# Optimization experiments

Hardware: AMD Instinct MI355X
Metric: run time of the kernel (lower is better)

## Reference

```python
import jax, jax.numpy as jnp
import numpy as np

NUM_Q = 100000; NUM_C = 1000; D = 128; BS = 128; SEQ = 128
QN = 4; CN = 10; NQC = 4; AGG_HOPS = 2; RANK_K = 10
NEG = jnp.float32(-1e9)


def setup_inputs() -> dict:
    key = jax.random.key(0)
    ks = iter(jax.random.split(key, 40))
    def nrm(shape, scale=0.05):
        return jax.random.normal(next(ks), shape, dtype=jnp.float32) * scale
    inp = {}
    inp['question_seq'] = jax.random.randint(next(ks), (BS, SEQ), 0, NUM_Q, dtype=jnp.int32)
    inp['correct_seq'] = jax.random.randint(next(ks), (BS, SEQ), 0, 2, dtype=jnp.int32)
    inp['mask_seq'] = jnp.ones((BS, SEQ), dtype=jnp.int32)
    inp['question_neighbors'] = jax.random.randint(next(ks), (NUM_Q, QN), 0, NUM_C, dtype=jnp.int32)
    inp['concept_neighbors'] = jax.random.randint(next(ks), (NUM_C, CN), 0, NUM_Q, dtype=jnp.int32)
    inp['qc_table'] = jax.random.randint(next(ks), (NUM_Q, NQC), 0, NUM_C, dtype=jnp.int32)
    inp['Eq'] = nrm((NUM_Q, D), 1.0)
    inp['Ec'] = nrm((NUM_C, D), 1.0)
    inp['Er'] = nrm((2, D), 1.0)
    inp['W_ih1'] = nrm((3 * D, 2 * D)); inp['W_hh1'] = nrm((3 * D, D))
    inp['b_ih1'] = nrm((3 * D,)); inp['b_hh1'] = nrm((3 * D,))
    inp['W_ih2'] = nrm((3 * D, D)); inp['W_hh2'] = nrm((3 * D, D))
    inp['b_ih2'] = nrm((3 * D,)); inp['b_hh2'] = nrm((3 * D,))
    inp['W_agg'] = nrm((AGG_HOPS, D, D)); inp['b_agg'] = nrm((AGG_HOPS, D))
    inp['W_agg_last'] = nrm((D, D)); inp['b_agg_last'] = nrm((D,))
    inp['Wq'] = nrm((D, D)); inp['bq'] = nrm((D,))
    inp['Wk'] = nrm((D, D)); inp['bk'] = nrm((D,))
    inp['Ww'] = nrm((1, 2 * D)); inp['bw'] = nrm((1,))
    inp['h1_init'] = nrm((BS, D)); inp['h2_init'] = nrm((BS, D))
    return inp


def _gru(x, h, W_ih, W_hh, b_ih, b_hh):
    gi = x @ W_ih.T + b_ih
    gh = h @ W_hh.T + b_hh
    ir, iz, i_n = jnp.split(gi, 3, axis=-1)
    hr, hz, hn = jnp.split(gh, 3, axis=-1)
    r = jax.nn.sigmoid(ir + hr)
    z = jax.nn.sigmoid(iz + hz)
    n = jnp.tanh(i_n + r * hn)
    return (1 - z) * n + z * h


def _forward(question_seq, correct_seq, mask_seq, question_neighbors, concept_neighbors, qc_table,
             Eq, Ec, Er, W_ih1, W_hh1, b_ih1, b_hh1, W_ih2, W_hh2, b_ih2, b_hh2,
             W_agg, b_agg, W_agg_last, b_agg_last, Wq, bq, Wk, bk, Ww, bw, h1_init, h2_init):
    bs, seq_len = question_seq.shape
    d = Eq.shape[1]
    # detached question embeddings of the whole history (recap scoring key)
    K_all = jax.lax.stop_gradient(Eq[question_seq])  # [bs, seq, d]
    Wh, Wqc = Ww[:, :d], Ww[:, d:]  # MLP_W split over [state; question_concept]

    def predict(qc, hist, hist_mask):
        # qc: [bs,nqc,d], hist: [bs,ns,d], hist_mask: [bs,ns]
        Kp = qc @ Wk.T + bk                     # MLP_key
        Qp = hist @ Wq.T + bq                   # MLP_query
        logits = jnp.einsum('bsd,bqd->bsq', Qp, Kp)
        logits = jnp.where(hist_mask[:, :, None], logits, NEG)
        w = jax.nn.softmax(logits.reshape(bs, -1), axis=1)
        # pairwise sigmoid(MLP_W([h; e])) without materializing the concat
        v = jax.nn.sigmoid((hist @ Wh[0])[:, :, None] + (qc @ Wqc[0])[:, None, :] + bw[0])
        return jnp.sum(w * v.reshape(bs, -1), axis=1)

    def step(carry, t):
        h1, h2, state_hist, y_hat = carry
        q_t = jnp.take(question_seq, t, axis=1)
        r_t = jnp.take(correct_seq, t, axis=1)
        m_t = jnp.take(mask_seq, t, axis=1) != 0
        # --- 2-hop GNN aggregation (question -> concept -> question) ---
        n1 = question_neighbors[q_t]            # [bs, QN] concept ids
        n2 = concept_neighbors[n1]              # [bs, QN, CN] question ids
        emb = [Eq[q_t], Ec[n1], Eq[n2]]
        for i in range(AGG_HOPS):
            for j in range(AGG_HOPS - i):
                s = jnp.mean(emb[j + 1], axis=-2) + emb[j]
                emb[j] = jnp.tanh(s @ W_agg[j].T + b_agg[j])
        agg = jnp.tanh(emb[0] @ W_agg_last.T + b_agg_last)
        emb_q = jnp.where(m_t[:, None], agg, Eq[q_t])
        # --- GRU state updates (dropout in eval mode = identity) ---
        h1n = _gru(jnp.concatenate([emb_q, Er[r_t]], axis=1), h1, W_ih1, W_hh1, b_ih1, b_hh1)
        g2 = _gru(h1n, h2, W_ih2, W_hh2, b_ih2, b_hh2)
        # --- next question + its concepts ---
        q_next = jnp.take(question_seq, t + 1, axis=1)
        qc = jnp.concatenate([Eq[q_next][:, None], Ec[qc_table[q_next]]], axis=1)  # [bs, 1+NQC, d]
        # --- soft recap: top-k history states by detached embedding similarity ---
        scores = jnp.einsum('bsd,bd->bs', K_all, jax.lax.stop_gradient(Eq[q_next]))
        valid = jnp.arange(seq_len) < t
        scores = jnp.where(valid[None, :], scores, NEG)
        top_vals, top_idx = jax.lax.top_k(scores, RANK_K)
        sel = jnp.take_along_axis(state_hist, top_idx[:, :, None], axis=1)  # [bs, k, d]
        sel_mask = top_vals > NEG / 2
        hist = jnp.concatenate([g2[:, None], sel], axis=1)
        hist_mask = jnp.concatenate([jnp.ones((bs, 1), dtype=bool), sel_mask], axis=1)
        p = predict(qc, hist, hist_mask)
        idx = jnp.where(t == 0, 0, t + 1)  # original writes y_hat[:,0] at t==0
        y_hat = y_hat.at[:, idx].set(p)
        # h2 / state_history NOT updated at t==0 (original `continue`)
        upd = t > 0
        h2n = jnp.where(upd, g2, h2)
        state_hist = jnp.where(upd, state_hist.at[:, t].set(g2), state_hist)
        return (h1n, h2n, state_hist, y_hat), None

    init = (h1_init, h2_init,
            jnp.zeros((bs, seq_len, d), jnp.float32),
            jnp.zeros((bs, seq_len), jnp.float32))
    (_, _, _, y_hat), _ = jax.lax.scan(jax.checkpoint(step), init, jnp.arange(seq_len - 1))
    return y_hat


def reference(question_seq, correct_seq, mask_seq, question_neighbors, concept_neighbors, qc_table,
              Eq, Ec, Er, W_ih1, W_hh1, b_ih1, b_hh1, W_ih2, W_hh2, b_ih2, b_hh2,
              W_agg, b_agg, W_agg_last, b_agg_last, Wq, bq, Wk, bk, Ww, bw, h1_init, h2_init):
    return _forward(question_seq, correct_seq, mask_seq, question_neighbors, concept_neighbors, qc_table,
                    Eq, Ec, Er, W_ih1, W_hh1, b_ih1, b_hh1, W_ih2, W_hh2, b_ih2, b_hh2,
                    W_agg, b_agg, W_agg_last, b_agg_last, Wq, bq, Wk, bk, Ww, bw, h1_init, h2_init)
```

## Files before the change

### kernel.cpp

```cpp
#include <hip/hip_runtime.h>

#define DD 128
#define BSZ 128
#define SEQL 128
#define TST 127
#define QNN 4
#define CNN 10
#define NQCC 4
#define RKK 10
#define NEGV -1000000000.0f

#define OFF_WTA0    0
#define OFF_WTA1    16384
#define OFF_WTAL    32768
#define OFF_WTIH1A  49152
#define OFF_ERIH1   98304
#define OFF_MT      99072
#define OFF_WPACK   115456
#define OFF_ECA0    189184
#define OFF_E1C     317184
#define OFF_KQC     445184
#define OFF_VQCC    509184
#define OFF_KBC     510184
#define OFF_U       511184
#define OFF_W2      511312
#define OFF_C0      511440
#define OFF_GRAM    511488
#define OFF_GI1     511488
#define OFF_KQ0     6753792
#define OFF_VQC0    7802368
#define OFF_KB0     7818752
#define OFF_TIX     7835136
#define OFF_TMSK    7997696
#define OFF_CID     8160256

#define XI(e) ((e) + (((e) >> 5) << 2))

typedef __fp16 h2 __attribute__((ext_vector_type(2)));

__device__ __forceinline__ float sigm(float x) { return 1.0f / (1.0f + __expf(-x)); }
__device__ __forceinline__ unsigned pkh(float a, float b) {
  h2 v; v.x = (__fp16)a; v.y = (__fp16)b;
  return __builtin_bit_cast(unsigned, v);
}
__device__ __forceinline__ float fd2(float acc, unsigned w, h2 x) {
  return __builtin_amdgcn_fdot2(__builtin_bit_cast(h2, w), x, acc, false);
}
__device__ __forceinline__ float fd2u(float acc, unsigned w, unsigned x) {
  return __builtin_amdgcn_fdot2(__builtin_bit_cast(h2, w), __builtin_bit_cast(h2, x), acc, false);
}
__device__ __forceinline__ void bar() {
  asm volatile("s_waitcnt lgkmcnt(0)" ::: "memory");
  __builtin_amdgcn_s_barrier();
  asm volatile("" ::: "memory");
}

__global__ __launch_bounds__(256) void k_prep(
    const float* __restrict__ W_hh1, const float* __restrict__ W_ih2,
    const float* __restrict__ W_hh2, const float* __restrict__ W_agg,
    const float* __restrict__ W_agg_last, const float* __restrict__ W_ih1,
    const float* __restrict__ Er, float* __restrict__ ws) {
  int idx = blockIdx.x * 256 + threadIdx.x;
  const int TOT = 172800;
  for (int o = idx; o < TOT; o += gridDim.x * 256) {
    int r = o;
    if (r < 16384) { int j = r >> 7, i = r & 127; ws[OFF_WTA0 + r] = W_agg[i * 128 + j]; continue; }
    r -= 16384;
    if (r < 16384) { int j = r >> 7, i = r & 127; ws[OFF_WTA1 + r] = W_agg[16384 + i * 128 + j]; continue; }
    r -= 16384;
    if (r < 16384) { int j = r >> 7, i = r & 127; ws[OFF_WTAL + r] = W_agg_last[i * 128 + j]; continue; }
    r -= 16384;
    if (r < 49152) { int j = r / 384, i = r % 384; ws[OFF_WTIH1A + r] = W_ih1[i * 256 + j]; continue; }
    r -= 49152;
    if (r < 768) {
      int rr = r / 384, i2 = r % 384;
      float a = 0.f;
      for (int j = 0; j < 128; ++j) a += Er[rr * 128 + j] * W_ih1[i2 * 256 + 128 + j];
      ws[OFF_ERIH1 + r] = a; continue;
    }
    r -= 768;
    {
      int n = r & 3; int q = r >> 2;
      int i = q & 127; q >>= 7;
      int kk = q & 3; q >>= 2;
      int jc = q & 3; int c = q >> 2;
      int j0 = jc * 32 + kk * 8 + n * 2;
      const float* row;
      if (c < 3) row = W_hh1 + (size_t)(c * 128 + i) * 128;
      else if (c < 6) row = W_ih2 + (size_t)((c - 3) * 128 + i) * 128;
      else row = W_hh2 + (size_t)((c - 6) * 128 + i) * 128;
      ((unsigned*)ws)[OFF_WPACK + r] = pkh(row[j0], row[j0 + 1]);
    }
  }
}

__global__ __launch_bounds__(128) void k_mqk(
    const float* __restrict__ Wq, const float* __restrict__ Wk,
    const float* __restrict__ bq, const float* __restrict__ bk,
    float* __restrict__ ws) {
  int j = blockIdx.x;
  int tid = threadIdx.x;
  if (j < 128) {
    __shared__ float wkc[128];
    wkc[tid] = Wk[tid * 128 + j];
    __syncthreads();
    float a = 0.f;
    for (int l = 0; l < 128; ++l) a = fmaf(Wq[l * 128 + tid], wkc[l], a);
    ws[OFF_MT + j * 128 + tid] = a;
  } else if (j == 128) {
    float a = 0.f;
    for (int l = 0; l < 128; ++l) a = fmaf(Wq[l * 128 + tid], bk[l], a);
    ws[OFF_U + tid] = a;
  } else {
    float a = 0.f;
    for (int l = 0; l < 128; ++l) a = fmaf(bq[l], Wk[l * 128 + tid], a);
    ws[OFF_W2 + tid] = a;
    __shared__ float sc[128];
    sc[tid] = bq[tid] * bk[tid];
    __syncthreads();
    if (tid == 0) { float s = 0.f; for (int l = 0; l < 128; ++l) s += sc[l]; ws[OFF_C0] = s; }
  }
}

__global__ __launch_bounds__(128) void k_concept(
    const int* __restrict__ cnbr, const float* __restrict__ Eq,
    const float* __restrict__ Ec, const float* __restrict__ b_agg,
    const float* __restrict__ Ww, float* __restrict__ ws) {
  int c = blockIdx.x;
  int tid = threadIdx.x;
  __shared__ int s_nb[CNN];
  __shared__ float s_v[DD], s_ec[DD], s_t2[DD], s_w2[DD], s_kb2[DD];
  if (tid < CNN) s_nb[tid] = cnbr[c * CNN + tid];
  __syncthreads();
  float ec = Ec[c * DD + tid];
  float cm = 0.f;
#pragma unroll
  for (int l = 0; l < CNN; ++l) cm += Eq[(size_t)s_nb[l] * DD + tid];
  s_ec[tid] = ec;
  s_v[tid] = cm * 0.1f + ec;
  __syncthreads();
  const float* WtA0 = ws + OFF_WTA0;
  const float* WtA1 = ws + OFF_WTA1;
  const float* MT = ws + OFF_MT;
  float a1 = 0.f, a0 = 0.f, kq = 0.f;
#pragma unroll 8
  for (int j = 0; j < DD; ++j) {
    a1 += WtA1[j * DD + tid] * s_v[j];
    a0 += WtA0[j * DD + tid] * s_ec[j];
    kq += MT[j * DD + tid] * s_ec[j];
  }
  ws[OFF_E1C + c * DD + tid] = tanhf(a1 + b_agg[DD + tid]);
  ws[OFF_ECA0 + c * DD + tid] = a0;
  s_t2[tid] = kq + ws[OFF_U + tid];
  s_w2[tid] = s_ec[tid] * Ww[128 + tid];
  s_kb2[tid] = s_ec[tid] * ws[OFF_W2 + tid];
  __syncthreads();
  if (tid < 64) {
    ((unsigned*)ws)[OFF_KQC + c * 64 + tid] = pkh(s_t2[2 * tid], s_t2[2 * tid + 1]);
    float pa = s_w2[tid] + s_w2[tid + 64];
    float pb = s_kb2[tid] + s_kb2[tid + 64];
    for (int off = 32; off > 0; off >>= 1) { pa += __shfl_down(pa, off); pb += __shfl_down(pb, off); }
    if (tid == 0) { ws[OFF_VQCC + c] = pa; ws[OFF_KBC + c] = pb + ws[OFF_C0]; }
  }
}

__global__ __launch_bounds__(256) void k_gram(
    const int* __restrict__ qseq, const float* __restrict__ Eq,
    const float* __restrict__ Ww, float* __restrict__ ws) {
  int b = blockIdx.x;
  int tid = threadIdx.x;
  __shared__ float sX[128][129];
  __shared__ float s_tmp[2][8][DD];
  __shared__ int sq[SEQL];
  __shared__ float sU[DD], sWqc[DD], sW2[DD];
  if (tid < 128) {
    sq[tid] = qseq[b * SEQL + tid];
    sU[tid] = ws[OFF_U + tid];
    sWqc[tid] = Ww[128 + tid];
    sW2[tid] = ws[OFF_W2 + tid];
  }
  __syncthreads();
  for (int o = tid; o < 128 * 32; o += 256) {
    int s = o >> 5, p = o & 31;
    float4 v = ((const float4*)(Eq + (size_t)sq[s] * DD))[p];
    sX[s][p * 4] = v.x; sX[s][p * 4 + 1] = v.y; sX[s][p * 4 + 2] = v.z; sX[s][p * 4 + 3] = v.w;
  }
  __syncthreads();
  {
    int r0 = (tid >> 4) * 8, c0 = (tid & 15) * 8;
    float acc[8][8];
#pragma unroll
    for (int u = 0; u < 8; ++u)
#pragma unroll
      for (int v = 0; v < 8; ++v) acc[u][v] = 0.f;
    for (int k = 0; k < 128; ++k) {
      float a[8], bb[8];
#pragma unroll
      for (int u = 0; u < 8; ++u) { a[u] = sX[r0 + u][k]; bb[u] = sX[c0 + u][k]; }
#pragma unroll
      for (int u = 0; u < 8; ++u)
#pragma unroll
        for (int v = 0; v < 8; ++v) acc[u][v] = fmaf(a[u], bb[v], acc[u][v]);
    }
    float* gb = ws + OFF_GRAM + (size_t)b * 16384;
#pragma unroll
    for (int u = 0; u < 8; ++u) {
      float4 v0 = {acc[u][0], acc[u][1], acc[u][2], acc[u][3]};
      float4 v1 = {acc[u][4], acc[u][5], acc[u][6], acc[u][7]};
      ((float4*)(gb + (size_t)(r0 + u) * 128 + c0))[0] = v0;
      ((float4*)(gb + (size_t)(r0 + u) * 128 + c0 + 4))[0] = v1;
    }
  }
  {
    const float* MT = ws + OFF_MT;
    unsigned* KQ0 = (unsigned*)ws + OFF_KQ0;
    int i = tid & 127, half = tid >> 7;
    int s0 = half * 64;
    for (int sb = 0; sb < 64; sb += 8) {
      float acc[8];
#pragma unroll
      for (int u = 0; u < 8; ++u) acc[u] = 0.f;
      for (int j = 0; j < DD; ++j) {
        float w = MT[j * DD + i];
#pragma unroll
        for (int u = 0; u < 8; ++u) acc[u] = fmaf(w, sX[s0 + sb + u][j], acc[u]);
      }
      __syncthreads();
#pragma unroll
      for (int u = 0; u < 8; ++u) s_tmp[half][u][i] = acc[u] + sU[i];
      __syncthreads();
      for (int o = tid; o < 16 * 64; o += 256) {
        int rr = o >> 6, e = o & 63;
        int hh = rr >> 3, uu = rr & 7;
        int s = hh * 64 + sb + uu;
        KQ0[((size_t)b * 128 + s) * 64 + e] = pkh(s_tmp[hh][uu][2 * e], s_tmp[hh][uu][2 * e + 1]);
      }
      __syncthreads();
    }
  }
  if (tid < 128) {
    float a = 0.f, kb = 0.f;
    for (int j = 0; j < DD; ++j) {
      float xv = sX[tid][j];
      a = fmaf(xv, sWqc[j], a);
      kb = fmaf(xv, sW2[j], kb);
    }
    ws[OFF_VQC0 + b * 128 + tid] = a;
    ws[OFF_KB0 + b * 128 + tid] = kb + ws[OFF_C0];
  }
}

__global__ __launch_bounds__(128) void k_topk(
    const int* __restrict__ qseq, const int* __restrict__ qctab,
    float* __restrict__ ws) {
  int* tix = (int*)(ws + OFF_TIX);
  int* tmsk = (int*)(ws + OFF_TMSK);
  int* cid = (int*)(ws + OFF_CID);
  int tid = threadIdx.x;
  int lane = tid & 63, wv = tid >> 6;
  int bt = blockIdx.x * 2 + wv;
  int b = bt / TST, t = bt - b * TST;
  if (lane < 5) {
    int qn = qseq[b * SEQL + t + 1];
    cid[(b * 128 + t + 1) * 5 + lane] = (lane == 0) ? qn : qctab[qn * NQCC + lane - 1];
  }
  const float* grow = ws + OFF_GRAM + ((size_t)b * 128 + (t + 1)) * 128;
  float v0 = (lane < t) ? grow[lane] : NEGV;
  float v1 = (lane + 64 < t) ? grow[lane + 64] : NEGV;
  for (int k = 0; k < RKK; ++k) {
    float bv = v0; int bi = lane;
    if (v1 > bv) { bv = v1; bi = lane + 64; }
    for (int off = 32; off > 0; off >>= 1) {
      float ov = __shfl_down(bv, off);
      int oi = __shfl_down(bi, off);
      if (ov > bv || (ov == bv && oi < bi)) { bv = ov; bi = oi; }
    }
    bv = __shfl(bv, 0); bi = __shfl(bi, 0);
    if (lane == 0) {
      tix[bt * RKK + k] = bi;
      tmsk[bt * RKK + k] = (bv > NEGV * 0.5f) ? 1 : 0;
    }
    if (bi == lane) v0 = -__builtin_inff();
    if (bi == lane + 64) v1 = -__builtin_inff();
  }
}

__global__ __launch_bounds__(128) void k_agg(
    const int* __restrict__ qseq, const int* __restrict__ rseq,
    const int* __restrict__ mseq, const int* __restrict__ qnbr,
    const float* __restrict__ Eq, const float* __restrict__ b_agg,
    const float* __restrict__ b_agg_last, const float* __restrict__ b_ih1,
    float* __restrict__ ws) {
  int blk = blockIdx.x;
  int b = blk >> 4, g = blk & 15;
  int t0 = g * 8;
  int nu = (t0 + 8 <= TST) ? 8 : (TST - t0);
  int tid = threadIdx.x;
  __shared__ float s_a[8][DD], s_b[8][DD], s_c[8][DD];
  __shared__ int s_q[8], s_r[8], s_m[8];
  __shared__ int s_n1[8][QNN];
  if (tid < 8) {
    int ok = tid < nu;
    int idx = b * SEQL + (ok ? (t0 + tid) : 0);
    s_q[tid] = qseq[idx];
    s_r[tid] = ok ? rseq[idx] : 0;
    s_m[tid] = ok ? mseq[idx] : 0;
  }
  __syncthreads();
  if (tid < 32) { int u = tid >> 2, k = tid & 3; s_n1[u][k] = qnbr[s_q[u] * QNN + k]; }
  for (int o = tid; o < 8 * 32; o += 128) {
    int u = o >> 5, p = o & 31;
    float4 v = ((const float4*)(Eq + (size_t)s_q[u] * DD))[p];
    s_a[u][p * 4] = v.x; s_a[u][p * 4 + 1] = v.y; s_a[u][p * 4 + 2] = v.z; s_a[u][p * 4 + 3] = v.w;
  }
  __syncthreads();
  const float* WtA0 = ws + OFF_WTA0;
  const float* WtAL = ws + OFF_WTAL;
  const float* WtIH1A = ws + OFF_WTIH1A;
  const float* EcA0 = ws + OFF_ECA0;
  const float* E1C = ws + OFF_E1C;
  float acc[8];
#pragma unroll
  for (int u = 0; u < 8; ++u) acc[u] = 0.f;
  for (int j = 0; j < DD; ++j) {
    float w = WtA0[j * DD + tid];
#pragma unroll
    for (int u = 0; u < 8; ++u) acc[u] = fmaf(w, s_a[u][j], acc[u]);
  }
  float bat = b_agg[tid];
#pragma unroll
  for (int u = 0; u < 8; ++u) {
    int n0 = s_n1[u][0], n1 = s_n1[u][1], n2 = s_n1[u][2], n3 = s_n1[u][3];
    float pre0 = 0.25f * (EcA0[n0 * DD + tid] + EcA0[n1 * DD + tid] + EcA0[n2 * DD + tid] + EcA0[n3 * DD + tid]);
    float e0 = tanhf(acc[u] + pre0 + bat);
    float e1m = 0.25f * (E1C[n0 * DD + tid] + E1C[n1 * DD + tid] + E1C[n2 * DD + tid] + E1C[n3 * DD + tid]);
    s_b[u][tid] = e1m + e0;
  }
  __syncthreads();
#pragma unroll
  for (int u = 0; u < 8; ++u) acc[u] = 0.f;
  for (int j = 0; j < DD; ++j) {
    float w = WtA0[j * DD + tid];
#pragma unroll
    for (int u = 0; u < 8; ++u) acc[u] = fmaf(w, s_b[u][j], acc[u]);
  }
#pragma unroll
  for (int u = 0; u < 8; ++u) s_c[u][tid] = tanhf(acc[u] + bat);
  __syncthreads();
#pragma unroll
  for (int u = 0; u < 8; ++u) acc[u] = 0.f;
  for (int j = 0; j < DD; ++j) {
    float w = WtAL[j * DD + tid];
#pragma unroll
    for (int u = 0; u < 8; ++u) acc[u] = fmaf(w, s_c[u][j], acc[u]);
  }
  float balt = b_agg_last[tid];
#pragma unroll
  for (int u = 0; u < 8; ++u) {
    float aggv = tanhf(acc[u] + balt);
    s_b[u][tid] = s_m[u] ? aggv : s_a[u][tid];
  }
  __syncthreads();
  float g0[8], g1[8], g2[8];
#pragma unroll
  for (int u = 0; u < 8; ++u) { g0[u] = 0.f; g1[u] = 0.f; g2[u] = 0.f; }
  for (int j = 0; j < DD; ++j) {
    float w0 = WtIH1A[j * 384 + tid];
    float w1 = WtIH1A[j * 384 + 128 + tid];
    float w2 = WtIH1A[j * 384 + 256 + tid];
#pragma unroll
    for (int u = 0; u < 8; ++u) {
      float x = s_b[u][j];
      g0[u] = fmaf(w0, x, g0[u]);
      g1[u] = fmaf(w1, x, g1[u]);
      g2[u] = fmaf(w2, x, g2[u]);
    }
  }
  for (int u = 0; u < nu; ++u) {
    const float* ErI = ws + OFF_ERIH1 + s_r[u] * 384;
    float* gi1 = ws + OFF_GI1 + (size_t)(b * TST + t0 + u) * 384;
    gi1[tid] = g0[u] + ErI[tid] + b_ih1[tid];
    gi1[128 + tid] = g1[u] + ErI[128 + tid] + b_ih1[128 + tid];
    gi1[256 + tid] = g2[u] + ErI[256 + tid] + b_ih1[256 + tid];
  }
}

__global__ __launch_bounds__(512, 2) void k_seq(
    const float* __restrict__ b_hh1, const float* __restrict__ b_ih2,
    const float* __restrict__ b_hh2, const float* __restrict__ Ww,
    const float* __restrict__ bw, const float* __restrict__ h1i,
    const float* __restrict__ h2i, float* __restrict__ ws,
    float* __restrict__ out) {
  const int tid = threadIdx.x;
  const int b = blockIdx.x;
  const int i = tid >> 2, jc = tid & 3;
  const int lane = tid & 63, wv = tid >> 6;
  const int bt0 = b * TST;

  const float4* gi1f4 = (const float4*)(ws + OFF_GI1);
  const unsigned* KQ0 = (const unsigned*)ws + OFF_KQ0;
  const unsigned* KQC = (const unsigned*)ws + OFF_KQC;
  const float* vqc0_all = ws + OFF_VQC0;
  const float* vqcC_all = ws + OFF_VQCC;
  const float* kb0_all = ws + OFF_KB0;
  const float* kbC_all = ws + OFF_KBC;
  const int* tix_all = (const int*)(ws + OFF_TIX);
  const int* tmsk_all = (const int*)(ws + OFF_TMSK);
  const int* cid_all = (const int*)(ws + OFF_CID);
  const uint4* wp = (const uint4*)((const unsigned*)ws + OFF_WPACK);

  __shared__ float s_h1[144], s_h2[144], s_h1n[144], s_g2[144];
  __shared__ unsigned qph_pk[SEQL * 66];
  __shared__ unsigned s_Kq[5 * 66];
  __shared__ float s_gi1[384];
  __shared__ float s_vhh[SEQL];
  __shared__ float s_logit[64];
  __shared__ float s_bhh1[384], s_bih2[384], s_bhh2[384];
  __shared__ float s_vh[11], s_vqc[2][5], s_kb[2][5], s_bw;
  __shared__ int s_tix[RKK], s_hm[11], s_cidn[5];

  uint4 wgt[9][4];
#pragma unroll
  for (int c = 0; c < 9; ++c)
#pragma unroll
    for (int kk = 0; kk < 4; ++kk)
      wgt[c][kk] = wp[((c * 4 + jc) * 4 + kk) * 128 + i];
#pragma unroll
  for (int c = 0; c < 9; ++c)
#pragma unroll
    for (int kk = 0; kk < 4; ++kk)
      asm volatile("" : "+v"(wgt[c][kk].x), "+v"(wgt[c][kk].y),
                        "+v"(wgt[c][kk].z), "+v"(wgt[c][kk].w));

  if (tid < 384) { s_bhh1[tid] = b_hh1[tid]; s_bih2[tid] = b_ih2[tid]; s_bhh2[tid] = b_hh2[tid]; }
  if (tid < 128) { s_h1[XI(tid)] = h1i[b * DD + tid]; s_h2[XI(tid)] = h2i[b * DD + tid]; s_vhh[tid] = 0.f; }
  if (tid >= 55 && tid < 64) s_logit[tid] = NEGV;
  float wh_lo = 0.f, wh_hi = 0.f;
  if (wv == 7) { wh_lo = Ww[lane]; wh_hi = Ww[64 + lane]; }
  if (tid == 0) { s_bw = bw[0]; out[b * SEQL + 1] = 0.f; s_hm[0] = 1; }
  if (tid >= 296 && tid < 301) s_cidn[tid - 296] = cid_all[(b * 128 + 1) * 5 + tid - 296];
  if (tid >= 304 && tid < 314) s_tix[tid - 304] = tix_all[bt0 * RKK + tid - 304];
  if (tid >= 320 && tid < 330) s_hm[1 + tid - 320] = tmsk_all[bt0 * RKK + tid - 320];
  __syncthreads();
  for (int o = tid; o < SEQL * 66; o += 512) qph_pk[o] = 0u;
  if (tid < 96) ((float4*)s_gi1)[tid] = gi1f4[(size_t)bt0 * 96 + tid];
  else if (tid < 256) {
    int kx = tid - 96;
    { int s = kx >> 6, e = kx & 63;
      s_Kq[s * 66 + e] = (s == 0) ? KQ0[(size_t)(b * 128 + 1) * 64 + e] : KQC[s_cidn[s] * 64 + e]; }
    { int kx2 = kx + 160; int s = kx2 >> 6, e = kx2 & 63;
      s_Kq[s * 66 + e] = KQC[s_cidn[s] * 64 + e]; }
  } else if (tid < 266) {
    int k = tid - 256;
    if (k < 5) s_vqc[0][k] = (k == 0) ? vqc0_all[b * 128 + 1] : vqcC_all[s_cidn[k]];
    else { int s = k - 5; s_kb[0][s] = (s == 0) ? kb0_all[b * 128 + 1] : kbC_all[s_cidn[s]]; }
  }
  __syncthreads();
  if (tid < 5) s_cidn[tid] = cid_all[(b * 128 + 2) * 5 + tid];
  __syncthreads();

  for (int t = 0; t < TST; ++t) {
    const int par = t & 1, parn = par ^ 1;
    const int tpn = (t + 1 < TST) ? t + 1 : TST - 1;
    const int tpp = (t + 2 < TST) ? t + 2 : TST - 1;
    float4 pf4 = {0.f, 0.f, 0.f, 0.f};
    unsigned pfu = 0, pfu2 = 0; int pfs = 0; float pfv = 0.f, pfkb = 0.f;

    if (tid < 96) pf4 = gi1f4[(size_t)(bt0 + tpn) * 96 + tid];
    else if (tid < 256) {
      int kx = tid - 96;
      { int s = kx >> 6, e = kx & 63;
        pfu = (s == 0) ? KQ0[(size_t)(b * 128 + tpn + 1) * 64 + e] : KQC[s_cidn[s] * 64 + e]; }
      { int kx2 = kx + 160; int s = kx2 >> 6, e = kx2 & 63;
        pfu2 = KQC[s_cidn[s] * 64 + e]; }
    } else if (tid < 291) {
      int k = tid - 256;
      if (k < 5) pfv = (k == 0) ? vqc0_all[b * 128 + tpn + 1] : vqcC_all[s_cidn[k]];
      else if (k < 10) { int s = k - 5; pfkb = (s == 0) ? kb0_all[b * 128 + tpn + 1] : kbC_all[s_cidn[s]]; }
      else if (k < 20) pfs = tix_all[(bt0 + tpn) * RKK + k - 10];
      else if (k < 30) pfs = tmsk_all[(bt0 + tpn) * RKK + k - 20];
      else pfs = cid_all[(b * 128 + tpp + 1) * 5 + k - 30];
    }
    {
      const float4* xp = (const float4*)s_h1 + jc * 9;
      float a0 = 0.f, a1 = 0.f, a2 = 0.f;
#pragma unroll
      for (int kk = 0; kk < 4; ++kk) {
        float4 x0 = xp[2 * kk], x1 = xp[2 * kk + 1];
        h2 p0 = __builtin_amdgcn_cvt_pkrtz(x0.x, x0.y);
        h2 p1 = __builtin_amdgcn_cvt_pkrtz(x0.z, x0.w);
        h2 p2 = __builtin_amdgcn_cvt_pkrtz(x1.x, x1.y);
        h2 p3 = __builtin_amdgcn_cvt_pkrtz(x1.z, x1.w);
        uint4 w;
        w = wgt[0][kk]; a0 = fd2(a0, w.x, p0); a0 = fd2(a0, w.y, p1); a0 = fd2(a0, w.z, p2); a0 = fd2(a0, w.w, p3);
        w = wgt[1][kk]; a1 = fd2(a1, w.x, p0); a1 = fd2(a1, w.y, p1); a1 = fd2(a1, w.z, p2); a1 = fd2(a1, w.w, p3);
        w = wgt[2][kk]; a2 = fd2(a2, w.x, p0); a2 = fd2(a2, w.y, p1); a2 = fd2(a2, w.z, p2); a2 = fd2(a2, w.w, p3);
      }
      a0 += __shfl_down(a0, 2); a0 += __shfl_down(a0, 1);
      a1 += __shfl_down(a1, 2); a1 += __shfl_down(a1, 1);
      a2 += __shfl_down(a2, 2); a2 += __shfl_down(a2, 1);
      if (jc == 0) {
        float r = sigm(s_gi1[i] + a0 + s_bhh1[i]);
        float z = sigm(s_gi1[128 + i] + a1 + s_bhh1[128 + i]);
        float n = tanhf(s_gi1[256 + i] + r * (a2 + s_bhh1[256 + i]));
        s_h1n[XI(i)] = (1.f - z) * n + z * s_h1[XI(i)];
      }
    }
    bar();

    {
      const float4* xn = (const float4*)s_h1n + jc * 9;
      const float4* xh = (const float4*)s_h2 + jc * 9;
      float a0 = 0.f, a1 = 0.f, a2 = 0.f, c0 = 0.f, c1 = 0.f, c2 = 0.f;
#pragma unroll
      for (int kk = 0; kk < 4; ++kk) {
        float4 n0 = xn[2 * kk], n1 = xn[2 * kk + 1];
        h2 p0 = __builtin_amdgcn_cvt_pkrtz(n0.x, n0.y);
        h2 p1 = __builtin_amdgcn_cvt_pkrtz(n0.z, n0.w);
        h2 p2 = __builtin_amdgcn_cvt_pkrtz(n1.x, n1.y);
        h2 p3 = __builtin_amdgcn_cvt_pkrtz(n1.z, n1.w);
        float4 h0 = xh[2 * kk], h1v = xh[2 * kk + 1];
        h2 q0 = __builtin_amdgcn_cvt_pkrtz(h0.x, h0.y);
        h2 q1 = __builtin_amdgcn_cvt_pkrtz(h0.z, h0.w);
        h2 q2 = __builtin_amdgcn_cvt_pkrtz(h1v.x, h1v.y);
        h2 q3 = __builtin_amdgcn_cvt_pkrtz(h1v.z, h1v.w);
        uint4 w;
        w = wgt[3][kk]; a0 = fd2(a0, w.x, p0); a0 = fd2(a0, w.y, p1); a0 = fd2(a0, w.z, p2); a0 = fd2(a0, w.w, p3);
        w = wgt[4][kk]; a1 = fd2(a1, w.x, p0); a1 = fd2(a1, w.y, p1); a1 = fd2(a1, w.z, p2); a1 = fd2(a1, w.w, p3);
        w = wgt[5][kk]; a2 = fd2(a2, w.x, p0); a2 = fd2(a2, w.y, p1); a2 = fd2(a2, w.z, p2); a2 = fd2(a2, w.w, p3);
        w = wgt[6][kk]; c0 = fd2(c0, w.x, q0); c0 = fd2(c0, w.y, q1); c0 = fd2(c0, w.z, q2); c0 = fd2(c0, w.w, q3);
        w = wgt[7][kk]; c1 = fd2(c1, w.x, q0); c1 = fd2(c1, w.y, q1); c1 = fd2(c1, w.z, q2); c1 = fd2(c1, w.w, q3);
        w = wgt[8][kk]; c2 = fd2(c2, w.x, q0); c2 = fd2(c2, w.y, q1); c2 = fd2(c2, w.z, q2); c2 = fd2(c2, w.w, q3);
      }
      a0 += __shfl_down(a0, 2); a0 += __shfl_down(a0, 1);
      a1 += __shfl_down(a1, 2); a1 += __shfl_down(a1, 1);
      a2 += __shfl_down(a2, 2); a2 += __shfl_down(a2, 1);
      c0 += __shfl_down(c0, 2); c0 += __shfl_down(c0, 1);
      c1 += __shfl_down(c1, 2); c1 += __shfl_down(c1, 1);
      c2 += __shfl_down(c2, 2); c2 += __shfl_down(c2, 1);
      if (jc == 0) {
        float r = sigm(a0 + s_bih2[i] + c0 + s_bhh2[i]);
        float z = sigm(a1 + s_bih2[128 + i] + c1 + s_bhh2[128 + i]);
        float n = tanhf(a2 + s_bih2[256 + i] + r * (c2 + s_bhh2[256 + i]));
        s_g2[XI(i)] = (1.f - z) * n + z * s_h2[XI(i)];
      }
    }
    bar();

    if (tid < 440) {
      int p = tid >> 3, sub = tid & 7;
      int q = p / 5, s = p - q * 5;
      const unsigned* kpr = &s_Kq[s * 66 + sub * 8];
      float a = 0.f;
      if (q == 0) {
        int e0 = sub * 16;
#pragma unroll
        for (int k = 0; k < 8; ++k) {
          int e = XI(e0 + 2 * k);
          h2 x = __builtin_amdgcn_cvt_pkrtz(s_g2[e], s_g2[e + 1]);
          a = fd2(a, kpr[k], x);
        }
      } else {
        const unsigned* ro = qph_pk + s_tix[q - 1] * 66;
#pragma unroll
        for (int k = 0; k < 8; ++k) a = fd2u(a, ro[sub * 8 + k], kpr[k]);
      }
      a += __shfl_down(a, 4);
      a += __shfl_down(a, 2);
      a += __shfl_down(a, 1);
      if (sub == 0) s_logit[p] = s_hm[q] ? (a + s_kb[par][s]) : NEGV;
    } else if (wv == 7) {
      float pa = s_g2[XI(lane)] * wh_lo + s_g2[XI(64 + lane)] * wh_hi;
      for (int off = 32; off > 0; off >>= 1) pa += __shfl_down(pa, off);
      if (lane == 0) s_vh[0] = pa;
      if (lane >= 16 && lane < 26) s_vh[1 + lane - 16] = s_vhh[s_tix[lane - 16]];
    }
    bar();

    if (wv == 7) {
      float l = s_logit[lane];
      float m = l;
      for (int off = 32; off > 0; off >>= 1) m = fmaxf(m, __shfl_xor(m, off));
      float e = __expf(l - m);
      float v = 0.f;
      if (lane < 55) {
        int q = lane / 5, s = lane - q * 5;
        v = sigm(s_vh[q] + s_vqc[par][s] + s_bw);
      }
      float num = e * v, den = e;
      for (int off = 32; off > 0; off >>= 1) { num += __shfl_xor(num, off); den += __shfl_xor(den, off); }
      if (lane == 0) out[b * SEQL + ((t == 0) ? 0 : (t + 1))] = num / den;
    } else {
      if (tid < 96) ((float4*)s_gi1)[tid] = pf4;
      else if (tid < 256) {
        int kx = tid - 96;
        { int s = kx >> 6, e = kx & 63; s_Kq[s * 66 + e] = pfu; }
        { int kx2 = kx + 160; int s = kx2 >> 6, e = kx2 & 63; s_Kq[s * 66 + e] = pfu2; }
      } else if (tid < 291) {
        int k = tid - 256;
        if (k < 5) s_vqc[parn][k] = pfv;
        else if (k < 10) s_kb[parn][k - 5] = pfkb;
        else if (k < 20) s_tix[k - 10] = pfs;
        else if (k < 30) s_hm[1 + k - 20] = pfs;
        else s_cidn[k - 30] = pfs;
      }
      if (tid >= 320 && tid < 448) {
        int ii = tid - 320;
        s_h1[XI(ii)] = s_h1n[XI(ii)];
        if (t > 0) s_h2[XI(ii)] = s_g2[XI(ii)];
      }
      if (t > 0 && tid >= 96 && tid < 160) {
        int k2 = tid - 96;
        int e = XI(2 * k2);
        qph_pk[t * 66 + k2] = pkh(s_g2[e], s_g2[e + 1]);
      }
      if (tid == 0 && t > 0) s_vhh[t] = s_vh[0];
    }
    bar();
  }
}

extern "C" void kernel_launch(void* const* d_in, const int* in_sizes, int n_in,
                              void* d_out, int out_size, void* d_ws, size_t ws_size,
                              hipStream_t stream) {
  (void)in_sizes; (void)n_in; (void)out_size; (void)ws_size;
  const int* qseq = (const int*)d_in[0];
  const int* rseq = (const int*)d_in[1];
  const int* mseq = (const int*)d_in[2];
  const int* qnbr = (const int*)d_in[3];
  const int* cnbr = (const int*)d_in[4];
  const int* qctab = (const int*)d_in[5];
  const float* Eq = (const float*)d_in[6];
  const float* Ec = (const float*)d_in[7];
  const float* Er = (const float*)d_in[8];
  const float* W_ih1 = (const float*)d_in[9];
  const float* W_hh1 = (const float*)d_in[10];
  const float* b_ih1 = (const float*)d_in[11];
  const float* b_hh1 = (const float*)d_in[12];
  const float* W_ih2 = (const float*)d_in[13];
  const float* W_hh2 = (const float*)d_in[14];
  const float* b_ih2 = (const float*)d_in[15];
  const float* b_hh2 = (const float*)d_in[16];
  const float* W_agg = (const float*)d_in[17];
  const float* b_agg = (const float*)d_in[18];
  const float* W_agg_last = (const float*)d_in[19];
  const float* b_agg_last = (const float*)d_in[20];
  const float* Wq = (const float*)d_in[21];
  const float* bq = (const float*)d_in[22];
  const float* Wk = (const float*)d_in[23];
  const float* bk = (const float*)d_in[24];
  const float* Ww = (const float*)d_in[25];
  const float* bw = (const float*)d_in[26];
  const float* h1i = (const float*)d_in[27];
  const float* h2i = (const float*)d_in[28];
  float* ws = (float*)d_ws;
  float* out = (float*)d_out;

  hipLaunchKernelGGL(k_prep, dim3(675), dim3(256), 0, stream,
                     W_hh1, W_ih2, W_hh2, W_agg, W_agg_last, W_ih1, Er, ws);
  hipLaunchKernelGGL(k_mqk, dim3(130), dim3(128), 0, stream,
                     Wq, Wk, bq, bk, ws);
  hipLaunchKernelGGL(k_concept, dim3(1000), dim3(128), 0, stream,
                     cnbr, Eq, Ec, b_agg, Ww, ws);
  hipLaunchKernelGGL(k_gram, dim3(BSZ), dim3(256), 0, stream,
                     qseq, Eq, Ww, ws);
  hipLaunchKernelGGL(k_topk, dim3(BSZ * TST / 2), dim3(128), 0, stream,
                     qseq, qctab, ws);
  hipLaunchKernelGGL(k_agg, dim3(BSZ * 16), dim3(128), 0, stream,
                     qseq, rseq, mseq, qnbr, Eq, b_agg, b_agg_last, b_ih1, ws);
  hipLaunchKernelGGL(k_seq, dim3(BSZ), dim3(512), 0, stream,
                     b_hh1, b_ih2, b_hh2, Ww, bw, h1i, h2i, ws, out);
}
```

Baseline: 655.6 us.

## Software-pipeline attention/readout stage one step behind GRU to drop a barrier

```diff
diff --git a/kernel.cpp b/kernel.cpp
--- a/kernel.cpp
+++ b/kernel.cpp
@@ -409,9 +409,10 @@
   const int* cid_all = (const int*)(ws + OFF_CID);
   const uint4* wp = (const uint4*)((const unsigned*)ws + OFF_WPACK);
 
-  __shared__ float s_h1[144], s_h2[144], s_h1n[144], s_g2[144];
+  __shared__ float s_h1[144], s_h2[144], s_h1n[144];
+  __shared__ float s_g2[2][144];
   __shared__ unsigned qph_pk[SEQL * 66];
-  __shared__ unsigned s_Kq[5 * 66];
+  __shared__ unsigned s_Kq[2][5 * 66];
   __shared__ float s_gi1[384];
   __shared__ float s_vhh[SEQL];
   __shared__ float s_logit[64];
@@ -439,49 +440,33 @@
   if (wv == 7) { wh_lo = Ww[lane]; wh_hi = Ww[64 + lane]; }
   if (tid == 0) { s_bw = bw[0]; out[b * SEQL + 1] = 0.f; s_hm[0] = 1; }
   if (tid >= 296 && tid < 301) s_cidn[tid - 296] = cid_all[(b * 128 + 1) * 5 + tid - 296];
-  if (tid >= 304 && tid < 314) s_tix[tid - 304] = tix_all[bt0 * RKK + tid - 304];
-  if (tid >= 320 && tid < 330) s_hm[1 + tid - 320] = tmsk_all[bt0 * RKK + tid - 320];
   __syncthreads();
   for (int o = tid; o < SEQL * 66; o += 512) qph_pk[o] = 0u;
   if (tid < 96) ((float4*)s_gi1)[tid] = gi1f4[(size_t)bt0 * 96 + tid];
-  else if (tid < 256) {
-    int kx = tid - 96;
-    { int s = kx >> 6, e = kx & 63;
-      s_Kq[s * 66 + e] = (s == 0) ? KQ0[(size_t)(b * 128 + 1) * 64 + e] : KQC[s_cidn[s] * 64 + e]; }
-    { int kx2 = kx + 160; int s = kx2 >> 6, e = kx2 & 63;
-      s_Kq[s * 66 + e] = KQC[s_cidn[s] * 64 + e]; }
-  } else if (tid < 266) {
-    int k = tid - 256;
-    if (k < 5) s_vqc[0][k] = (k == 0) ? vqc0_all[b * 128 + 1] : vqcC_all[s_cidn[k]];
-    else { int s = k - 5; s_kb[0][s] = (s == 0) ? kb0_all[b * 128 + 1] : kbC_all[s_cidn[s]]; }
-  }
-  __syncthreads();
-  if (tid < 5) s_cidn[tid] = cid_all[(b * 128 + 2) * 5 + tid];
-  __syncthreads();
-
-  for (int t = 0; t < TST; ++t) {
+  __syncthreads();
+
+  for (int t = 0; t <= TST; ++t) {
     const int par = t & 1, parn = par ^ 1;
-    const int tpn = (t + 1 < TST) ? t + 1 : TST - 1;
-    const int tpp = (t + 2 < TST) ? t + 2 : TST - 1;
     float4 pf4 = {0.f, 0.f, 0.f, 0.f};
     unsigned pfu = 0, pfu2 = 0; int pfs = 0; float pfv = 0.f, pfkb = 0.f;
 
-    if (tid < 96) pf4 = gi1f4[(size_t)(bt0 + tpn) * 96 + tid];
-    else if (tid < 256) {
-      int kx = tid - 96;
-      { int s = kx >> 6, e = kx & 63;
-        pfu = (s == 0) ? KQ0[(size_t)(b * 128 + tpn + 1) * 64 + e] : KQC[s_cidn[s] * 64 + e]; }
-      { int kx2 = kx + 160; int s = kx2 >> 6, e = kx2 & 63;
-        pfu2 = KQC[s_cidn[s] * 64 + e]; }
-    } else if (tid < 291) {
-      int k = tid - 256;
-      if (k < 5) pfv = (k == 0) ? vqc0_all[b * 128 + tpn + 1] : vqcC_all[s_cidn[k]];
-      else if (k < 10) { int s = k - 5; pfkb = (s == 0) ? kb0_all[b * 128 + tpn + 1] : kbC_all[s_cidn[s]]; }
-      else if (k < 20) pfs = tix_all[(bt0 + tpn) * RKK + k - 10];
-      else if (k < 30) pfs = tmsk_all[(bt0 + tpn) * RKK + k - 20];
-      else pfs = cid_all[(b * 128 + tpp + 1) * 5 + k - 30];
-    }
-    {
+    if (t < TST) {
+      const int tg = (t + 1 < TST) ? t + 1 : TST - 1;
+      if (tid < 96) pf4 = gi1f4[(size_t)(bt0 + tg) * 96 + tid];
+      else if (tid < 256) {
+        int kx = tid - 96;
+        { int s = kx >> 6, e = kx & 63;
+          pfu = (s == 0) ? KQ0[(size_t)(b * 128 + t + 1) * 64 + e] : KQC[s_cidn[s] * 64 + e]; }
+        { int kx2 = kx + 160; int s = kx2 >> 6, e = kx2 & 63;
+          pfu2 = KQC[s_cidn[s] * 64 + e]; }
+      } else if (tid < 291) {
+        int k = tid - 256;
+        if (k < 5) pfv = (k == 0) ? vqc0_all[b * 128 + t + 1] : vqcC_all[s_cidn[k]];
+        else if (k < 10) { int s = k - 5; pfkb = (s == 0) ? kb0_all[b * 128 + t + 1] : kbC_all[s_cidn[s]]; }
+        else if (k < 20) pfs = tix_all[(bt0 + t) * RKK + k - 10];
+        else if (k < 30) pfs = tmsk_all[(bt0 + t) * RKK + k - 20];
+        else { int tn = (t + 1 < TST) ? t + 1 : TST - 1; pfs = cid_all[(b * 128 + tn + 1) * 5 + k - 30]; }
+      }
       const float4* xp = (const float4*)s_h1 + jc * 9;
       float a0 = 0.f, a1 = 0.f, a2 = 0.f;
 #pragma unroll
@@ -506,11 +491,42 @@
         s_h1n[XI(i)] = (1.f - z) * n + z * s_h1[XI(i)];
       }
     }
+    if (t >= 1) {
+      if (tid < 440) {
+        int p = tid >> 3, sub = tid & 7;
+        int q = p / 5, s = p - q * 5;
+        const unsigned* kpr = &s_Kq[parn][s * 66 + sub * 8];
+        float a = 0.f;
+        if (q == 0) {
+          int e0 = sub * 16;
+#pragma unroll
+          for (int k = 0; k < 8; ++k) {
+            int e = XI(e0 + 2 * k);
+            h2 x = __builtin_amdgcn_cvt_pkrtz(s_g2[parn][e], s_g2[parn][e + 1]);
+            a = fd2(a, kpr[k], x);
+          }
+        } else {
+          const unsigned* ro = qph_pk + s_tix[q - 1] * 66;
+#pragma unroll
+          for (int k = 0; k < 8; ++k) a = fd2u(a, ro[sub * 8 + k], kpr[k]);
+        }
+        a += __shfl_down(a, 4);
+        a += __shfl_down(a, 2);
+        a += __shfl_down(a, 1);
+        if (sub == 0) s_logit[p] = s_hm[q] ? (a + s_kb[parn][s]) : NEGV;
+      } else if (wv == 7) {
+        float pa = s_g2[parn][XI(lane)] * wh_lo + s_g2[parn][XI(64 + lane)] * wh_hi;
+        for (int off = 32; off > 0; off >>= 1) pa += __shfl_down(pa, off);
+        if (lane == 0) s_vh[0] = pa;
+        if (lane >= 16 && lane < 26) s_vh[1 + lane - 16] = s_vhh[s_tix[lane - 16]];
+      }
+    }
     bar();
 
-    {
+    if (t < TST) {
       const float4* xn = (const float4*)s_h1n + jc * 9;
-      const float4* xh = (const float4*)s_h2 + jc * 9;
+      const float4* xh = (t <= 1) ? ((const float4*)s_h2 + jc * 9)
+                                  : ((const float4*)s_g2[parn] + jc * 9);
       float a0 = 0.f, a1 = 0.f, a2 = 0.f, c0 = 0.f, c1 = 0.f, c2 = 0.f;
 #pragma unroll
       for (int kk = 0; kk < 4; ++kk) {
@@ -542,42 +558,11 @@
         float r = sigm(a0 + s_bih2[i] + c0 + s_bhh2[i]);
         float z = sigm(a1 + s_bih2[128 + i] + c1 + s_bhh2[128 + i]);
         float n = tanhf(a2 + s_bih2[256 + i] + r * (c2 + s_bhh2[256 + i]));
-        s_g2[XI(i)] = (1.f - z) * n + z * s_h2[XI(i)];
-      }
-    }
-    bar();
-
-    if (tid < 440) {
-      int p = tid >> 3, sub = tid & 7;
-      int q = p / 5, s = p - q * 5;
-      const unsigned* kpr = &s_Kq[s * 66 + sub * 8];
-      float a = 0.f;
-      if (q == 0) {
-        int e0 = sub * 16;
-#pragma unroll
-        for (int k = 0; k < 8; ++k) {
-          int e = XI(e0 + 2 * k);
-          h2 x = __builtin_amdgcn_cvt_pkrtz(s_g2[e], s_g2[e + 1]);
-          a = fd2(a, kpr[k], x);
-        }
-      } else {
-        const unsigned* ro = qph_pk + s_tix[q - 1] * 66;
-#pragma unroll
-        for (int k = 0; k < 8; ++k) a = fd2u(a, ro[sub * 8 + k], kpr[k]);
-      }
-      a += __shfl_down(a, 4);
-      a += __shfl_down(a, 2);
-      a += __shfl_down(a, 1);
-      if (sub == 0) s_logit[p] = s_hm[q] ? (a + s_kb[par][s]) : NEGV;
-    } else if (wv == 7) {
-      float pa = s_g2[XI(lane)] * wh_lo + s_g2[XI(64 + lane)] * wh_hi;
-      for (int off = 32; off > 0; off >>= 1) pa += __shfl_down(pa, off);
-      if (lane == 0) s_vh[0] = pa;
-      if (lane >= 16 && lane < 26) s_vh[1 + lane - 16] = s_vhh[s_tix[lane - 16]];
-    }
-    bar();
-
-    if (wv == 7) {
+        float h2old = (t <= 1) ? s_h2[XI(i)] : s_g2[parn][XI(i)];
+        s_g2[par][XI(i)] = (1.f - z) * n + z * h2old;
+      }
+    }
+    if (t >= 1 && wv == 7) {
       float l = s_logit[lane];
       float m = l;
       for (int off = 32; off > 0; off >>= 1) m = fmaxf(m, __shfl_xor(m, off));
@@ -585,21 +570,22 @@
       float v = 0.f;
       if (lane < 55) {
         int q = lane / 5, s = lane - q * 5;
-        v = sigm(s_vh[q] + s_vqc[par][s] + s_bw);
+        v = sigm(s_vh[q] + s_vqc[parn][s] + s_bw);
       }
       float num = e * v, den = e;
       for (int off = 32; off > 0; off >>= 1) { num += __shfl_xor(num, off); den += __shfl_xor(den, off); }
-      if (lane == 0) out[b * SEQL + ((t == 0) ? 0 : (t + 1))] = num / den;
-    } else {
+      if (lane == 0) out[b * SEQL + ((t - 1 == 0) ? 0 : t)] = num / den;
+    }
+    if (t < TST) {
       if (tid < 96) ((float4*)s_gi1)[tid] = pf4;
       else if (tid < 256) {
         int kx = tid - 96;
-        { int s = kx >> 6, e = kx & 63; s_Kq[s * 66 + e] = pfu; }
-        { int kx2 = kx + 160; int s = kx2 >> 6, e = kx2 & 63; s_Kq[s * 66 + e] = pfu2; }
+        { int s = kx >> 6, e = kx & 63; s_Kq[par][s * 66 + e] = pfu; }
+        { int kx2 = kx + 160; int s = kx2 >> 6, e = kx2 & 63; s_Kq[par][s * 66 + e] = pfu2; }
       } else if (tid < 291) {
         int k = tid - 256;
-        if (k < 5) s_vqc[parn][k] = pfv;
-        else if (k < 10) s_kb[parn][k - 5] = pfkb;
+        if (k < 5) s_vqc[par][k] = pfv;
+        else if (k < 10) s_kb[par][k - 5] = pfkb;
         else if (k < 20) s_tix[k - 10] = pfs;
         else if (k < 30) s_hm[1 + k - 20] = pfs;
         else s_cidn[k - 30] = pfs;
@@ -607,15 +593,14 @@
       if (tid >= 320 && tid < 448) {
         int ii = tid - 320;
         s_h1[XI(ii)] = s_h1n[XI(ii)];
-        if (t > 0) s_h2[XI(ii)] = s_g2[XI(ii)];
-      }
-      if (t > 0 && tid >= 96 && tid < 160) {
-        int k2 = tid - 96;
-        int e = XI(2 * k2);
-        qph_pk[t * 66 + k2] = pkh(s_g2[e], s_g2[e + 1]);
-      }
-      if (tid == 0 && t > 0) s_vhh[t] = s_vh[0];
-    }
+      }
+    }
+    if (t >= 2 && tid >= 96 && tid < 160) {
+      int k2 = tid - 96;
+      int e = XI(2 * k2);
+      qph_pk[(t - 1) * 66 + k2] = pkh(s_g2[parn][e], s_g2[parn][e + 1]);
+    }
+    if (t >= 2 && tid == 0) s_vhh[t - 1] = s_vh[0];
     bar();
   }
 }
```

Result: faster. 624.4 us (-4.8%).
